# Kernel optimization log

Hardware: AMD Instinct MI355X
Metric: run time of the kernel (lower is better)

## Reference

```python
import math
import jax, jax.numpy as jnp
import numpy as np

NT, NS, B, D, V = 128, 128, 8, 512, 32000


def setup_inputs() -> dict:
    key = jax.random.key(0)
    ks = jax.random.split(key, 9)
    s = 0.02
    return {
        "htgt": jax.random.normal(ks[0], (NT, B, D), jnp.float32),
        "hsrc": jax.random.normal(ks[1], (NS, B, D), jnp.float32),
        "src": jax.random.randint(ks[2], (NS, B), 0, V),
        "Wq": jax.random.normal(ks[3], (D, D), jnp.float32) * s,
        "bq": jnp.zeros((D,), jnp.float32),
        "Wf": jax.random.normal(ks[4], (D, D), jnp.float32) * s,
        "bf": jnp.zeros((D,), jnp.float32),
        "Wg": jax.random.normal(ks[5], (D, V), jnp.float32) * s,
        "bg": jnp.zeros((V,), jnp.float32),
        "Wc": jax.random.normal(ks[6], (D, 1), jnp.float32) * s,
        "bc": jnp.zeros((1,), jnp.float32),
    }


def reference(htgt, hsrc, src, Wq, bq, Wf, bf, Wg, bg, Wc, bc):
    Nt, bs, d = htgt.shape
    vocab = Wg.shape[1]
    # generator logits: (Nt,B,V) -> (B,Nt,V)
    p_gen = (jnp.einsum('tbd,dv->tbv', htgt, Wg) + bg).transpose(1, 0, 2)
    # single-head attention; NOTE: original code projects q, k, v all with q_proj
    q = (htgt @ Wq + bq).transpose(1, 0, 2) / math.sqrt(d)   # (B,Nt,D)
    k = (hsrc @ Wq + bq).transpose(1, 0, 2)                  # (B,Ns,D)
    v = (hsrc @ Wq + bq).transpose(1, 0, 2)                  # (B,Ns,D)
    attn = jax.nn.softmax(jnp.einsum('btd,bsd->bts', q, k), axis=-1)  # (B,Nt,Ns)
    x = jnp.einsum('bts,bsd->btd', attn, v)                  # (B,Nt,D)
    scores = x @ Wf + bf                                     # (B,Nt,D)
    # copy gate: sum over target positions (original sums dim 0 of (Nt,B,D))
    a_copy = jax.nn.sigmoid(scores.sum(axis=1) @ Wc + bc)    # (B,1)
    a_copy = a_copy[:, :, None]                              # (B,1,1)
    # scatter-add attention probs into vocab buckets (replaces one-hot bmm)
    def scat(attn_b, src_b):
        return jnp.zeros((attn_b.shape[0], vocab), attn_b.dtype).at[:, src_b].add(attn_b)
    p_copy = jax.vmap(scat)(attn, src.T)                     # (B,Nt,V)
    res = a_copy * p_copy + (1.0 - a_copy) * p_gen           # (B,Nt,V)
    return res.transpose(1, 0, 2)                            # (Nt,B,V)
```

## Files before the change

kernel.cpp:

```cpp
#include <hip/hip_runtime.h>
#include <math.h>

#define NTt 128
#define NSs 128
#define BB  8
#define DD  512
#define VV  32000

typedef unsigned short ushortT;
typedef unsigned int uintT;
__device__ __forceinline__ ushortT f2bf(float x) {
    uintT u = __float_as_uint(x);
    u = (u + 0x7fffu + ((u >> 16) & 1u)) >> 16;
    return (ushortT)u;
}
__device__ __forceinline__ float bf2f(ushortT h) {
    return __uint_as_float(((uintT)h) << 16);
}

typedef __attribute__((ext_vector_type(8))) short bf16x8;
typedef __attribute__((ext_vector_type(4))) float f32x4;

#define GLL16(g, l) __builtin_amdgcn_global_load_lds(                          \
    (const __attribute__((address_space(1))) unsigned int*)(g),                \
    (__attribute__((address_space(3))) unsigned int*)(l), 16, 0, 0)

#define LDSC 4096

__global__ __launch_bounds__(256)
void prep_kernel(const float* __restrict__ Wg, const float* __restrict__ htgt,
                 const float* __restrict__ Wf, const float* __restrict__ Wc,
                 ushortT* __restrict__ Bpack, ushortT* __restrict__ Apack,
                 float* __restrict__ wfc) {
    const int bx = blockIdx.x;
    const int tid = threadIdx.x;
    if (bx < 4000) {
        __shared__ float tile[32][129];
        const int p = bx >> 4, t = bx & 15;
        const int n0 = p * 128, k0 = t * 32;
#pragma unroll
        for (int i = 0; i < 4; ++i) {
            const int idx = tid + i * 256;
            const int row = idx >> 5;
            const int c4 = (idx & 31) * 4;
            float4 v = *(const float4*)(Wg + (size_t)(k0 + row) * VV + n0 + c4);
            tile[row][c4 + 0] = v.x; tile[row][c4 + 1] = v.y;
            tile[row][c4 + 2] = v.z; tile[row][c4 + 3] = v.w;
        }
        __syncthreads();
        const int r = tid >> 1;
        const int c2 = tid & 1;
        uintT h[16], l[16];
#pragma unroll
        for (int j = 0; j < 16; ++j) {
            const float x = tile[c2 * 16 + j][r];
            h[j] = f2bf(x);
            l[j] = f2bf(x - bf2f((ushortT)h[j]));
        }
        ushortT* dh = Bpack + ((size_t)(p * 16 + t) * 2 + 0) * LDSC + r * 32 + c2 * 16;
        ushortT* dl = Bpack + ((size_t)(p * 16 + t) * 2 + 1) * LDSC + r * 32 + c2 * 16;
        uint4 hv0, hv1, lv0, lv1;
        hv0.x = h[0] | (h[1] << 16);  hv0.y = h[2] | (h[3] << 16);
        hv0.z = h[4] | (h[5] << 16);  hv0.w = h[6] | (h[7] << 16);
        hv1.x = h[8] | (h[9] << 16);  hv1.y = h[10] | (h[11] << 16);
        hv1.z = h[12] | (h[13] << 16); hv1.w = h[14] | (h[15] << 16);
        lv0.x = l[0] | (l[1] << 16);  lv0.y = l[2] | (l[3] << 16);
        lv0.z = l[4] | (l[5] << 16);  lv0.w = l[6] | (l[7] << 16);
        lv1.x = l[8] | (l[9] << 16);  lv1.y = l[10] | (l[11] << 16);
        lv1.z = l[12] | (l[13] << 16); lv1.w = l[14] | (l[15] << 16);
        *(uint4*)dh = hv0; *(uint4*)(dh + 8) = hv1;
        *(uint4*)dl = lv0; *(uint4*)(dl + 8) = lv1;
    } else if (bx < 4128) {
        const int idx = bx - 4000;
        const int p = idx >> 4, t = idx & 15;
        const int r = tid >> 1, c2 = tid & 1;
        const float* srcp = htgt + (size_t)(p * 128 + r) * DD + t * 32 + c2 * 16;
        uintT h[16], l[16];
#pragma unroll
        for (int q = 0; q < 4; ++q) {
            float4 v = *(const float4*)(srcp + q * 4);
            float xs[4] = {v.x, v.y, v.z, v.w};
#pragma unroll
            for (int j = 0; j < 4; ++j) {
                const int e = q * 4 + j;
                h[e] = f2bf(xs[j]);
                l[e] = f2bf(xs[j] - bf2f((ushortT)h[e]));
            }
        }
        ushortT* dh = Apack + ((size_t)(p * 16 + t) * 2 + 0) * LDSC + r * 32 + c2 * 16;
        ushortT* dl = Apack + ((size_t)(p * 16 + t) * 2 + 1) * LDSC + r * 32 + c2 * 16;
        uint4 hv0, hv1, lv0, lv1;
        hv0.x = h[0] | (h[1] << 16);  hv0.y = h[2] | (h[3] << 16);
        hv0.z = h[4] | (h[5] << 16);  hv0.w = h[6] | (h[7] << 16);
        hv1.x = h[8] | (h[9] << 16);  hv1.y = h[10] | (h[11] << 16);
        hv1.z = h[12] | (h[13] << 16); hv1.w = h[14] | (h[15] << 16);
        lv0.x = l[0] | (l[1] << 16);  lv0.y = l[2] | (l[3] << 16);
        lv0.z = l[4] | (l[5] << 16);  lv0.w = l[6] | (l[7] << 16);
        lv1.x = l[8] | (l[9] << 16);  lv1.y = l[10] | (l[11] << 16);
        lv1.z = l[12] | (l[13] << 16); lv1.w = l[14] | (l[15] << 16);
        *(uint4*)dh = hv0; *(uint4*)(dh + 8) = hv1;
        *(uint4*)dl = lv0; *(uint4*)(dl + 8) = lv1;
    } else {
        __shared__ float sWc[DD];
        sWc[tid] = Wc[tid];
        sWc[tid + 256] = Wc[tid + 256];
        __syncthreads();
        const int w = tid >> 6, lane = tid & 63;
        const int row = (bx - 4128) * 4 + w;
        const float* rp = Wf + (size_t)row * DD + lane * 8;
        float4 a = *(const float4*)rp;
        float4 b = *(const float4*)(rp + 4);
        const float* c = &sWc[lane * 8];
        float s = a.x * c[0] + a.y * c[1] + a.z * c[2] + a.w * c[3]
                + b.x * c[4] + b.y * c[5] + b.z * c[6] + b.w * c[7];
        for (int off = 32; off; off >>= 1) s += __shfl_xor(s, off);
        if (lane == 0) wfc[row] = s;
    }
}

#define QBM 64
#define QBN 64
#define QBK 16
__global__ __launch_bounds__(256)
void qkv_gemm(const float* __restrict__ htgt, const float* __restrict__ hsrc,
              const float* __restrict__ Wq, const float* __restrict__ bq,
              float* __restrict__ QK) {
    __shared__ float As[QBK][QBM];
    __shared__ float Bs[QBK][QBN];
    const int m0 = blockIdx.x * QBM;
    const int n0 = blockIdx.y * QBN;
    const int tid = threadIdx.x;
    const int tx = tid & 15, ty = tid >> 4;
    const float* Abase = (m0 < 1024) ? (htgt + (size_t)m0 * DD)
                                     : (hsrc + (size_t)(m0 - 1024) * DD);
    float acc[4][4];
#pragma unroll
    for (int i = 0; i < 4; ++i)
#pragma unroll
        for (int j = 0; j < 4; ++j) acc[i][j] = 0.f;

    const int ar = tid >> 2;
    const int ak = (tid & 3) * 4;
    const int br = tid >> 4;
    const int bc4 = (tid & 15) * 4;

    for (int k0 = 0; k0 < DD; k0 += QBK) {
        float4 av = *(const float4*)(Abase + (size_t)ar * DD + k0 + ak);
        float4 bv = *(const float4*)(Wq + (size_t)(k0 + br) * DD + n0 + bc4);
        As[ak + 0][ar] = av.x; As[ak + 1][ar] = av.y;
        As[ak + 2][ar] = av.z; As[ak + 3][ar] = av.w;
        *(float4*)&Bs[br][bc4] = bv;
        __syncthreads();
#pragma unroll
        for (int kk = 0; kk < QBK; ++kk) {
            float4 a4 = *(const float4*)&As[kk][ty * 4];
            float4 b4 = *(const float4*)&Bs[kk][tx * 4];
            float a[4] = {a4.x, a4.y, a4.z, a4.w};
            float b[4] = {b4.x, b4.y, b4.z, b4.w};
#pragma unroll
            for (int i = 0; i < 4; ++i)
#pragma unroll
                for (int j = 0; j < 4; ++j)
                    acc[i][j] = fmaf(a[i], b[j], acc[i][j]);
        }
        __syncthreads();
    }
    const float scale = (m0 < 1024) ? 0.044194173824159216f : 1.0f;
    float4 bqv = *(const float4*)&bq[n0 + tx * 4];
#pragma unroll
    for (int i = 0; i < 4; ++i) {
        const int m = m0 + ty * 4 + i;
        float4 o;
        o.x = (acc[i][0] + bqv.x) * scale;
        o.y = (acc[i][1] + bqv.y) * scale;
        o.z = (acc[i][2] + bqv.z) * scale;
        o.w = (acc[i][3] + bqv.w) * scale;
        *(float4*)&QK[(size_t)m * DD + n0 + tx * 4] = o;
    }
}

__global__ __launch_bounds__(256)
void attn_kernel(const float* __restrict__ QK, float* __restrict__ attn) {
    const int b = blockIdx.x & 7;
    const int tpair = blockIdx.x >> 3;
    const int tid = threadIdx.x;
    const int h = tid >> 7;
    const int s = tid & 127;
    const int t = tpair * 2 + h;
    __shared__ float sQ[2][DD];
    __shared__ float sred[8];
    *(float4*)&sQ[h][s * 4] = *(const float4*)&QK[(size_t)(t * BB + b) * DD + s * 4];
    __syncthreads();
    const float* Krow = QK + (size_t)(1024 + s * BB + b) * DD;
    const float* q = &sQ[h][0];
    float4 accv = make_float4(0.f, 0.f, 0.f, 0.f);
    for (int d = 0; d < DD; d += 4) {
        float4 kv = *(const float4*)(Krow + d);
        accv.x = fmaf(kv.x, q[d + 0], accv.x);
        accv.y = fmaf(kv.y, q[d + 1], accv.y);
        accv.z = fmaf(kv.z, q[d + 2], accv.z);
        accv.w = fmaf(kv.w, q[d + 3], accv.w);
    }
    const float dot = accv.x + accv.y + accv.z + accv.w;
    float m = dot;
    for (int off = 32; off; off >>= 1) m = fmaxf(m, __shfl_xor(m, off));
    const int wv = tid >> 6;
    if ((tid & 63) == 0) sred[wv] = m;
    __syncthreads();
    m = fmaxf(sred[h * 2], sred[h * 2 + 1]);
    const float p = __expf(dot - m);
    float ssum = p;
    for (int off = 32; off; off >>= 1) ssum += __shfl_xor(ssum, off);
    __syncthreads();
    if ((tid & 63) == 0) sred[4 + wv] = ssum;
    __syncthreads();
    ssum = sred[4 + h * 2] + sred[4 + h * 2 + 1];
    attn[(size_t)(b * NTt + t) * NSs + s] = p / ssum;
}

__global__ __launch_bounds__(128)
void acopy_kernel(const float* __restrict__ QK, const float* __restrict__ wfc,
                  const float* __restrict__ attn, const float* __restrict__ bf,
                  const float* __restrict__ Wc, const float* __restrict__ bc,
                  float* __restrict__ ac) {
    const int b = blockIdx.x;
    const int tid = threadIdx.x;
    __shared__ float sW[DD];
    __shared__ float sred[4];
    *(float4*)&sW[tid * 4] = *(const float4*)&wfc[tid * 4];
    __syncthreads();
    float cs = 0.f;
    const float* arow = attn + (size_t)b * NTt * NSs + tid;
#pragma unroll 4
    for (int tq = 0; tq < NTt; ++tq) cs += arow[(size_t)tq * NSs];
    const float* Krow = QK + (size_t)(1024 + tid * BB + b) * DD;
    float4 accv = make_float4(0.f, 0.f, 0.f, 0.f);
    for (int d = 0; d < DD; d += 4) {
        float4 kv = *(const float4*)(Krow + d);
        accv.x = fmaf(kv.x, sW[d + 0], accv.x);
        accv.y = fmaf(kv.y, sW[d + 1], accv.y);
        accv.z = fmaf(kv.z, sW[d + 2], accv.z);
        accv.w = fmaf(kv.w, sW[d + 3], accv.w);
    }
    const float kw = accv.x + accv.y + accv.z + accv.w;
    float val = cs * kw;
    float cw = 0.f;
#pragma unroll
    for (int j = 0; j < 4; ++j) cw += bf[tid + j * 128] * Wc[tid + j * 128];
    for (int off = 32; off; off >>= 1) {
        val += __shfl_xor(val, off);
        cw  += __shfl_xor(cw, off);
    }
    if ((tid & 63) == 0) { sred[tid >> 6] = val; sred[2 + (tid >> 6)] = cw; }
    __syncthreads();
    if (tid == 0) {
        const float z = sred[0] + sred[1] + (float)NTt * (sred[2] + sred[3]) + bc[0];
        ac[b] = 1.0f / (1.0f + __expf(-z));
    }
}

__global__ __launch_bounds__(256)
void pgen_mfma(const ushortT* __restrict__ Apack, const ushortT* __restrict__ Bpack,
               const float* __restrict__ bg, const float* __restrict__ ac,
               float* __restrict__ out) {
    __shared__ __align__(16) ushortT sT[4 * LDSC];
    __shared__ float s_ac[8];

    const int idx = blockIdx.x;
    const int wg  = (idx & 7) * 250 + (idx >> 3);
    const int nb  = wg >> 3;
    const int mb  = wg & 7;
    const int m0 = mb * 128;
    const int n0 = nb * 128;

    const int tid = threadIdx.x;
    const int wid = tid >> 6;
    const int lane = tid & 63;
    const int wm = wid >> 1, wn = wid & 1;
    const int g = lane >> 4;
    const int lr = lane & 15;

    if (tid < 8) s_ac[tid] = 1.0f - ac[tid];

    const ushortT* gsrc = ((wid < 2) ? (Apack + (size_t)mb * 16 * 2 * LDSC)
                                     : (Bpack + (size_t)nb * 16 * 2 * LDSC))
                          + (size_t)(wid & 1) * LDSC;
    ushortT* ldst = &sT[wid * LDSC];

    f32x4 acc[4][4];
#pragma unroll
    for (int i = 0; i < 4; ++i)
#pragma unroll
        for (int j = 0; j < 4; ++j) acc[i][j] = (f32x4){0.f, 0.f, 0.f, 0.f};

    for (int t = 0; t < 16; ++t) {
#pragma unroll
        for (int i = 0; i < 8; ++i) {
            GLL16(gsrc + i * 512 + lane * 8, ldst + i * 512);
        }
        __syncthreads();

        bf16x8 fah[4], fal[4], fbh[4], fbl[4];
#pragma unroll
        for (int i = 0; i < 4; ++i) {
            const int arow = wm * 64 + i * 16 + lr;
            const int brow = wn * 64 + i * 16 + lr;
            fah[i] = *(const bf16x8*)&sT[0 * LDSC + arow * 32 + g * 8];
            fal[i] = *(const bf16x8*)&sT[1 * LDSC + arow * 32 + g * 8];
            fbh[i] = *(const bf16x8*)&sT[2 * LDSC + brow * 32 + g * 8];
            fbl[i] = *(const bf16x8*)&sT[3 * LDSC + brow * 32 + g * 8];
        }
#pragma unroll
        for (int mi = 0; mi < 4; ++mi)
#pragma unroll
            for (int ni = 0; ni < 4; ++ni) {
                acc[mi][ni] = __builtin_amdgcn_mfma_f32_16x16x32_bf16(
                    fah[mi], fbh[ni], acc[mi][ni], 0, 0, 0);
                acc[mi][ni] = __builtin_amdgcn_mfma_f32_16x16x32_bf16(
                    fah[mi], fbl[ni], acc[mi][ni], 0, 0, 0);
                acc[mi][ni] = __builtin_amdgcn_mfma_f32_16x16x32_bf16(
                    fal[mi], fbh[ni], acc[mi][ni], 0, 0, 0);
            }
        __syncthreads();
        gsrc += 2 * LDSC;
    }

    float bgv[4];
#pragma unroll
    for (int i = 0; i < 4; ++i) bgv[i] = bg[n0 + wn * 64 + i * 16 + lr];
#pragma unroll
    for (int mi = 0; mi < 4; ++mi) {
#pragma unroll
        for (int r = 0; r < 4; ++r) {
            const int m = m0 + wm * 64 + mi * 16 + g * 4 + r;
            const float s = s_ac[(g * 4 + r) & 7];
            const size_t ob = (size_t)m * VV + n0 + wn * 64 + lr;
#pragma unroll
            for (int ni = 0; ni < 4; ++ni) {
                out[ob + ni * 16] = s * (acc[mi][ni][r] + bgv[ni]);
            }
        }
    }
}

#define BM 128
#define BN 128
#define BK 8
__global__ __launch_bounds__(256)
void pgen_gemm(const float* __restrict__ htgt, const float* __restrict__ Wg,
               const float* __restrict__ bg, const float* __restrict__ ac,
               float* __restrict__ out) {
    __shared__ float As[BK][BM];
    __shared__ float Bs[BK][BN];
    const int m0 = blockIdx.x * BM;
    const int n0 = blockIdx.y * BN;
    const int tid = threadIdx.x;
    const int tx = tid & 15, ty = tid >> 4;
    const float* Abase = htgt + (size_t)m0 * DD;
    float acc[8][8];
#pragma unroll
    for (int i = 0; i < 8; ++i)
#pragma unroll
        for (int j = 0; j < 8; ++j) acc[i][j] = 0.f;
    const int ar = tid >> 1;
    const int ah = (tid & 1) * 4;
    const int bk = tid >> 5;
    const int bj = (tid & 31) * 4;
    for (int k0 = 0; k0 < DD; k0 += BK) {
        float4 av = *(const float4*)(Abase + (size_t)ar * DD + k0 + ah);
        float4 bv = *(const float4*)(Wg + (size_t)(k0 + bk) * VV + n0 + bj);
        As[ah + 0][ar] = av.x; As[ah + 1][ar] = av.y;
        As[ah + 2][ar] = av.z; As[ah + 3][ar] = av.w;
        *(float4*)&Bs[bk][bj] = bv;
        __syncthreads();
#pragma unroll
        for (int kk = 0; kk < BK; ++kk) {
            float4 a0 = *(const float4*)&As[kk][ty * 8];
            float4 a1 = *(const float4*)&As[kk][ty * 8 + 4];
            float4 b0 = *(const float4*)&Bs[kk][tx * 8];
            float4 b1 = *(const float4*)&Bs[kk][tx * 8 + 4];
            float a[8] = {a0.x, a0.y, a0.z, a0.w, a1.x, a1.y, a1.z, a1.w};
            float b[8] = {b0.x, b0.y, b0.z, b0.w, b1.x, b1.y, b1.z, b1.w};
#pragma unroll
            for (int i = 0; i < 8; ++i)
#pragma unroll
                for (int j = 0; j < 8; ++j)
                    acc[i][j] = fmaf(a[i], b[j], acc[i][j]);
        }
        __syncthreads();
    }
    float sc[8];
#pragma unroll
    for (int i = 0; i < 8; ++i) sc[i] = 1.0f - ac[i];
#pragma unroll
    for (int i = 0; i < 8; ++i) {
        const int m = m0 + ty * 8 + i;
        const float s = sc[i];
#pragma unroll
        for (int j = 0; j < 8; j += 4) {
            const int n = n0 + tx * 8 + j;
            float4 o;
            o.x = s * (acc[i][j + 0] + bg[n + 0]);
            o.y = s * (acc[i][j + 1] + bg[n + 1]);
            o.z = s * (acc[i][j + 2] + bg[n + 2]);
            o.w = s * (acc[i][j + 3] + bg[n + 3]);
            *(float4*)&out[(size_t)m * VV + n] = o;
        }
    }
}

__global__ __launch_bounds__(256)
void scatter_kernel(const float* __restrict__ attn, const float* __restrict__ ac,
                    const int* __restrict__ src, float* __restrict__ out) {
    const int gid = blockIdx.x * 256 + threadIdx.x;
    const int b = gid >> 14;
    const int rem = gid & 16383;
    const int t = rem >> 7;
    const int s = rem & 127;
    const float a = ac[b];
    const int v = src[s * BB + b];
    atomicAdd(&out[(size_t)(t * BB + b) * VV + v],
              a * attn[(size_t)(b * NTt + t) * NSs + s]);
}

extern "C" void kernel_launch(void* const* d_in, const int* in_sizes, int n_in,
                              void* d_out, int out_size, void* d_ws, size_t ws_size,
                              hipStream_t stream) {
    (void)in_sizes; (void)n_in; (void)out_size;
    const float* htgt = (const float*)d_in[0];
    const float* hsrc = (const float*)d_in[1];
    const int*   src  = (const int*)d_in[2];
    const float* Wq   = (const float*)d_in[3];
    const float* bq   = (const float*)d_in[4];
    const float* Wf   = (const float*)d_in[5];
    const float* bf   = (const float*)d_in[6];
    const float* Wg   = (const float*)d_in[7];
    const float* bg   = (const float*)d_in[8];
    const float* Wc   = (const float*)d_in[9];
    const float* bc   = (const float*)d_in[10];
    float* out = (float*)d_out;

    float* ws   = (float*)d_ws;
    float* QK   = ws;
    float* attn = QK + 2048 * 512;
    float* wfc  = attn + 131072;
    float* ac   = wfc + 512;

    size_t fp32_bytes = (size_t)(1048576 + 131072 + 512 + 16) * 4;
    size_t base2 = (fp32_bytes + 255) & ~(size_t)255;
    ushortT* Apack = (ushortT*)((char*)d_ws + base2);
    ushortT* Bpack = Apack + (size_t)8 * 16 * 2 * LDSC;
    size_t need = base2 + ((size_t)8 * 16 * 2 * LDSC + (size_t)250 * 16 * 2 * LDSC) * 2;

    const bool use_mfma = (ws_size >= need);
    if (use_mfma) {
        prep_kernel<<<4256, 256, 0, stream>>>(Wg, htgt, Wf, Wc, Bpack, Apack, wfc);
    } else {
        prep_kernel<<<dim3(128), 256, 0, stream>>>(Wg, htgt, Wf, Wc,
                                                   (ushortT*)ws, (ushortT*)ws, wfc);
    }
    qkv_gemm<<<dim3(32, 8), 256, 0, stream>>>(htgt, hsrc, Wq, bq, QK);
    attn_kernel<<<512, 256, 0, stream>>>(QK, attn);
    acopy_kernel<<<8, 128, 0, stream>>>(QK, wfc, attn, bf, Wc, bc, ac);

    if (use_mfma) {
        pgen_mfma<<<2000, 256, 0, stream>>>(Apack, Bpack, bg, ac, out);
    } else {
        pgen_gemm<<<dim3(8, 250), 256, 0, stream>>>(htgt, Wg, bg, ac, out);
    }
    scatter_kernel<<<512, 256, 0, stream>>>(attn, ac, src, out);
}
```

Measured before the change: 411.3 us.

## Double-buffer pgen LDS tiles and pack operands in MFMA fragment order

The pgen MFMA GEMM now keeps two LDS buffers and issues the global-to-LDS load for the next K tile before computing on the current one, so each iteration needs one barrier instead of two. The prep kernel now writes the bf16 hi/lo packs in per-lane fragment order, so each wave reads its fragments with contiguous lane*8 LDS accesses instead of row-strided ones, which may reduce bank conflicts. The fallback path gets a dedicated wfc-only kernel instead of an incorrect prep_kernel launch. Doubling LDS to 64 KB per block may lower occupancy.

```diff
diff --git a/kernel.cpp b/kernel.cpp
--- a/kernel.cpp
+++ b/kernel.cpp
@@ -26,6 +26,7 @@
     (__attribute__((address_space(3))) unsigned int*)(l), 16, 0, 0)
 
 #define LDSC 4096
+
 
 __global__ __launch_bounds__(256)
 void prep_kernel(const float* __restrict__ Wg, const float* __restrict__ htgt,
@@ -48,58 +49,58 @@
             tile[row][c4 + 2] = v.z; tile[row][c4 + 3] = v.w;
         }
         __syncthreads();
-        const int r = tid >> 1;
-        const int c2 = tid & 1;
-        uintT h[16], l[16];
-#pragma unroll
-        for (int j = 0; j < 16; ++j) {
-            const float x = tile[c2 * 16 + j][r];
-            h[j] = f2bf(x);
-            l[j] = f2bf(x - bf2f((ushortT)h[j]));
-        }
-        ushortT* dh = Bpack + ((size_t)(p * 16 + t) * 2 + 0) * LDSC + r * 32 + c2 * 16;
-        ushortT* dl = Bpack + ((size_t)(p * 16 + t) * 2 + 1) * LDSC + r * 32 + c2 * 16;
-        uint4 hv0, hv1, lv0, lv1;
-        hv0.x = h[0] | (h[1] << 16);  hv0.y = h[2] | (h[3] << 16);
-        hv0.z = h[4] | (h[5] << 16);  hv0.w = h[6] | (h[7] << 16);
-        hv1.x = h[8] | (h[9] << 16);  hv1.y = h[10] | (h[11] << 16);
-        hv1.z = h[12] | (h[13] << 16); hv1.w = h[14] | (h[15] << 16);
-        lv0.x = l[0] | (l[1] << 16);  lv0.y = l[2] | (l[3] << 16);
-        lv0.z = l[4] | (l[5] << 16);  lv0.w = l[6] | (l[7] << 16);
-        lv1.x = l[8] | (l[9] << 16);  lv1.y = l[10] | (l[11] << 16);
-        lv1.z = l[12] | (l[13] << 16); lv1.w = l[14] | (l[15] << 16);
-        *(uint4*)dh = hv0; *(uint4*)(dh + 8) = hv1;
-        *(uint4*)dl = lv0; *(uint4*)(dl + 8) = lv1;
+        const size_t cb = ((size_t)(p * 16 + t) * 2) * LDSC;
+#pragma unroll
+        for (int h2 = 0; h2 < 2; ++h2) {
+            const int pgi = h2 * 256 + tid;
+            const int fi  = pgi >> 6;
+            const int gg  = (pgi >> 4) & 3;
+            const int lr2 = pgi & 15;
+            const int row = fi * 16 + lr2;
+            uintT h[8], l[8];
+#pragma unroll
+            for (int j = 0; j < 8; ++j) {
+                const float x = tile[gg * 8 + j][row];
+                h[j] = f2bf(x);
+                l[j] = f2bf(x - bf2f((ushortT)h[j]));
+            }
+            uint4 hv, lv;
+            hv.x = h[0] | (h[1] << 16); hv.y = h[2] | (h[3] << 16);
+            hv.z = h[4] | (h[5] << 16); hv.w = h[6] | (h[7] << 16);
+            lv.x = l[0] | (l[1] << 16); lv.y = l[2] | (l[3] << 16);
+            lv.z = l[4] | (l[5] << 16); lv.w = l[6] | (l[7] << 16);
+            *(uint4*)(Bpack + cb + (size_t)pgi * 8) = hv;
+            *(uint4*)(Bpack + cb + LDSC + (size_t)pgi * 8) = lv;
+        }
     } else if (bx < 4128) {
-        const int idx = bx - 4000;
-        const int p = idx >> 4, t = idx & 15;
-        const int r = tid >> 1, c2 = tid & 1;
-        const float* srcp = htgt + (size_t)(p * 128 + r) * DD + t * 32 + c2 * 16;
-        uintT h[16], l[16];
-#pragma unroll
-        for (int q = 0; q < 4; ++q) {
-            float4 v = *(const float4*)(srcp + q * 4);
-            float xs[4] = {v.x, v.y, v.z, v.w};
-#pragma unroll
-            for (int j = 0; j < 4; ++j) {
-                const int e = q * 4 + j;
-                h[e] = f2bf(xs[j]);
-                l[e] = f2bf(xs[j] - bf2f((ushortT)h[e]));
+        const int idx2 = bx - 4000;
+        const int p = idx2 >> 4, t = idx2 & 15;
+        const size_t cb = ((size_t)(p * 16 + t) * 2) * LDSC;
+#pragma unroll
+        for (int h2 = 0; h2 < 2; ++h2) {
+            const int pgi = h2 * 256 + tid;
+            const int fi  = pgi >> 6;
+            const int gg  = (pgi >> 4) & 3;
+            const int lr2 = pgi & 15;
+            const int row = fi * 16 + lr2;
+            const float* srcp = htgt + (size_t)(p * 128 + row) * DD + t * 32 + gg * 8;
+            float4 v0 = *(const float4*)srcp;
+            float4 v1 = *(const float4*)(srcp + 4);
+            float xs[8] = {v0.x, v0.y, v0.z, v0.w, v1.x, v1.y, v1.z, v1.w};
+            uintT h[8], l[8];
+#pragma unroll
+            for (int j = 0; j < 8; ++j) {
+                h[j] = f2bf(xs[j]);
+                l[j] = f2bf(xs[j] - bf2f((ushortT)h[j]));
             }
-        }
-        ushortT* dh = Apack + ((size_t)(p * 16 + t) * 2 + 0) * LDSC + r * 32 + c2 * 16;
-        ushortT* dl = Apack + ((size_t)(p * 16 + t) * 2 + 1) * LDSC + r * 32 + c2 * 16;
-        uint4 hv0, hv1, lv0, lv1;
-        hv0.x = h[0] | (h[1] << 16);  hv0.y = h[2] | (h[3] << 16);
-        hv0.z = h[4] | (h[5] << 16);  hv0.w = h[6] | (h[7] << 16);
-        hv1.x = h[8] | (h[9] << 16);  hv1.y = h[10] | (h[11] << 16);
-        hv1.z = h[12] | (h[13] << 16); hv1.w = h[14] | (h[15] << 16);
-        lv0.x = l[0] | (l[1] << 16);  lv0.y = l[2] | (l[3] << 16);
-        lv0.z = l[4] | (l[5] << 16);  lv0.w = l[6] | (l[7] << 16);
-        lv1.x = l[8] | (l[9] << 16);  lv1.y = l[10] | (l[11] << 16);
-        lv1.z = l[12] | (l[13] << 16); lv1.w = l[14] | (l[15] << 16);
-        *(uint4*)dh = hv0; *(uint4*)(dh + 8) = hv1;
-        *(uint4*)dl = lv0; *(uint4*)(dl + 8) = lv1;
+            uint4 hv, lv;
+            hv.x = h[0] | (h[1] << 16); hv.y = h[2] | (h[3] << 16);
+            hv.z = h[4] | (h[5] << 16); hv.w = h[6] | (h[7] << 16);
+            lv.x = l[0] | (l[1] << 16); lv.y = l[2] | (l[3] << 16);
+            lv.z = l[4] | (l[5] << 16); lv.w = l[6] | (l[7] << 16);
+            *(uint4*)(Apack + cb + (size_t)pgi * 8) = hv;
+            *(uint4*)(Apack + cb + LDSC + (size_t)pgi * 8) = lv;
+        }
     } else {
         __shared__ float sWc[DD];
         sWc[tid] = Wc[tid];
@@ -116,6 +117,26 @@
         for (int off = 32; off; off >>= 1) s += __shfl_xor(s, off);
         if (lane == 0) wfc[row] = s;
     }
+}
+
+__global__ __launch_bounds__(256)
+void wfc_only_kernel(const float* __restrict__ Wf, const float* __restrict__ Wc,
+                     float* __restrict__ wfc) {
+    __shared__ float sWc[DD];
+    const int tid = threadIdx.x;
+    sWc[tid] = Wc[tid];
+    sWc[tid + 256] = Wc[tid + 256];
+    __syncthreads();
+    const int w = tid >> 6, lane = tid & 63;
+    const int row = blockIdx.x * 4 + w;
+    const float* rp = Wf + (size_t)row * DD + lane * 8;
+    float4 a = *(const float4*)rp;
+    float4 b = *(const float4*)(rp + 4);
+    const float* c = &sWc[lane * 8];
+    float s = a.x * c[0] + a.y * c[1] + a.z * c[2] + a.w * c[3]
+            + b.x * c[4] + b.y * c[5] + b.z * c[6] + b.w * c[7];
+    for (int off = 32; off; off >>= 1) s += __shfl_xor(s, off);
+    if (lane == 0) wfc[row] = s;
 }
 
 #define QBM 64
@@ -263,7 +284,7 @@
 void pgen_mfma(const ushortT* __restrict__ Apack, const ushortT* __restrict__ Bpack,
                const float* __restrict__ bg, const float* __restrict__ ac,
                float* __restrict__ out) {
-    __shared__ __align__(16) ushortT sT[4 * LDSC];
+    __shared__ __align__(16) ushortT sT[2][4 * LDSC];
     __shared__ float s_ac[8];
 
     const int idx = blockIdx.x;
@@ -282,10 +303,11 @@
 
     if (tid < 8) s_ac[tid] = 1.0f - ac[tid];
 
-    const ushortT* gsrc = ((wid < 2) ? (Apack + (size_t)mb * 16 * 2 * LDSC)
-                                     : (Bpack + (size_t)nb * 16 * 2 * LDSC))
-                          + (size_t)(wid & 1) * LDSC;
-    ushortT* ldst = &sT[wid * LDSC];
+    const ushortT* gs = ((wid < 2) ? (Apack + (size_t)mb * 16 * 2 * LDSC)
+                                   : (Bpack + (size_t)nb * 16 * 2 * LDSC))
+                        + (size_t)(wid & 1) * LDSC;
+    ushortT* ld0 = &sT[0][wid * LDSC];
+    ushortT* ld1 = &sT[1][wid * LDSC];
 
     f32x4 acc[4][4];
 #pragma unroll
@@ -293,22 +315,20 @@
 #pragma unroll
         for (int j = 0; j < 4; ++j) acc[i][j] = (f32x4){0.f, 0.f, 0.f, 0.f};
 
-    for (int t = 0; t < 16; ++t) {
-#pragma unroll
-        for (int i = 0; i < 8; ++i) {
-            GLL16(gsrc + i * 512 + lane * 8, ldst + i * 512);
-        }
-        __syncthreads();
-
+    auto step = [&](const ushortT* Bp, ushortT* nxt, bool stage) {
+        if (stage) {
+#pragma unroll
+            for (int i = 0; i < 8; ++i)
+                GLL16(gs + i * 512 + lane * 8, nxt + i * 512);
+            gs += 2 * LDSC;
+        }
         bf16x8 fah[4], fal[4], fbh[4], fbl[4];
 #pragma unroll
         for (int i = 0; i < 4; ++i) {
-            const int arow = wm * 64 + i * 16 + lr;
-            const int brow = wn * 64 + i * 16 + lr;
-            fah[i] = *(const bf16x8*)&sT[0 * LDSC + arow * 32 + g * 8];
-            fal[i] = *(const bf16x8*)&sT[1 * LDSC + arow * 32 + g * 8];
-            fbh[i] = *(const bf16x8*)&sT[2 * LDSC + brow * 32 + g * 8];
-            fbl[i] = *(const bf16x8*)&sT[3 * LDSC + brow * 32 + g * 8];
+            fah[i] = *(const bf16x8*)&Bp[0 * LDSC + (wm * 4 + i) * 512 + lane * 8];
+            fal[i] = *(const bf16x8*)&Bp[1 * LDSC + (wm * 4 + i) * 512 + lane * 8];
+            fbh[i] = *(const bf16x8*)&Bp[2 * LDSC + (wn * 4 + i) * 512 + lane * 8];
+            fbl[i] = *(const bf16x8*)&Bp[3 * LDSC + (wn * 4 + i) * 512 + lane * 8];
         }
 #pragma unroll
         for (int mi = 0; mi < 4; ++mi)
@@ -322,7 +342,17 @@
                     fal[mi], fbh[ni], acc[mi][ni], 0, 0, 0);
             }
         __syncthreads();
-        gsrc += 2 * LDSC;
+    };
+
+#pragma unroll
+    for (int i = 0; i < 8; ++i)
+        GLL16(gs + i * 512 + lane * 8, ld0 + i * 512);
+    gs += 2 * LDSC;
+    __syncthreads();
+
+    for (int tp = 0; tp < 8; ++tp) {
+        step(&sT[0][0], ld1, true);
+        step(&sT[1][0], ld0, tp < 7);
     }
 
     float bgv[4];
@@ -456,8 +486,7 @@
     if (use_mfma) {
         prep_kernel<<<4256, 256, 0, stream>>>(Wg, htgt, Wf, Wc, Bpack, Apack, wfc);
     } else {
-        prep_kernel<<<dim3(128), 256, 0, stream>>>(Wg, htgt, Wf, Wc,
-                                                   (ushortT*)ws, (ushortT*)ws, wfc);
+        wfc_only_kernel<<<128, 256, 0, stream>>>(Wf, Wc, wfc);
     }
     qkv_gemm<<<dim3(32, 8), 256, 0, stream>>>(htgt, hsrc, Wq, bq, QK);
     attn_kernel<<<512, 256, 0, stream>>>(QK, attn);
```

Result: faster. 396.3 us (-3.7%).
